# Optimization experiments

Hardware: AMD Instinct MI355X
Metric: run time of the kernel (lower is better)

Reference implementation:

```python
import jax, jax.numpy as jnp
import numpy as np

EPS = 1e-8  # torch.nn.CosineSimilarity default eps


def setup_inputs() -> dict:
    key = jax.random.key(0)
    k1, k2 = jax.random.split(key)
    B, C, D = 16384, 2048, 1024
    inputs = jax.random.normal(k1, (B, D), dtype=jnp.float32)
    class_avgs = jax.random.normal(k2, (C, D), dtype=jnp.float32)
    return {"inputs": inputs, "class_avgs": class_avgs}


def reference(inputs, class_avgs):
    # Pairwise cosine similarity: out[b, c] = <x_b, a_c> / (max(||x_b||, eps) * max(||a_c||, eps))
    x_norm = jnp.maximum(jnp.linalg.norm(inputs, axis=-1, keepdims=True), EPS)      # [B, 1]
    a_norm = jnp.maximum(jnp.linalg.norm(class_avgs, axis=-1, keepdims=True), EPS)  # [C, 1]
    xn = inputs / x_norm          # [B, D]
    an = class_avgs / a_norm      # [C, D]
    return jnp.einsum('bd,cd->bc', xn, an)  # [B, C]
```

## Files before the change

kernel.cpp:

```cpp
#include <hip/hip_runtime.h>
#include <stdint.h>


#define D_DIM 1024
#define N_DIM 2048
#define BMt 256
#define BNt 256
#define BKt 128
#define NKT 8

typedef int   i32x4 __attribute__((ext_vector_type(4)));
typedef float f32x4 __attribute__((ext_vector_type(4)));

__global__ __launch_bounds__(256) void quant_rows(
        const float* __restrict__ x, const float* __restrict__ a,
        char* __restrict__ xq, char* __restrict__ aq,
        float* __restrict__ sx, float* __restrict__ sa, int Bn) {
    const int blk = blockIdx.x;
    const float* in = (blk < Bn) ? x : a;
    char* outq      = (blk < Bn) ? xq : aq;
    float* outs     = (blk < Bn) ? sx : sa;
    const int row = (blk < Bn) ? blk : blk - Bn;
    const int t = threadIdx.x;
    const float4 v = ((const float4*)(in + (size_t)row * D_DIM))[t];
    float ss = v.x * v.x + v.y * v.y + v.z * v.z + v.w * v.w;
    float mx = fmaxf(fmaxf(fabsf(v.x), fabsf(v.y)), fmaxf(fabsf(v.z), fabsf(v.w)));
#pragma unroll
    for (int o = 1; o < 64; o <<= 1) {
        ss += __shfl_xor(ss, o);
        mx = fmaxf(mx, __shfl_xor(mx, o));
    }
    __shared__ float redS[4], redM[4];
    if ((t & 63) == 0) { redS[t >> 6] = ss; redM[t >> 6] = mx; }
    __syncthreads();
    const float tot  = redS[0] + redS[1] + redS[2] + redS[3];
    const float amax = fmaxf(fmaxf(redM[0], redM[1]), fmaxf(redM[2], redM[3]));
    const float inv  = (amax > 0.0f) ? (127.0f / amax) : 0.0f;
    int q0 = __float2int_rn(v.x * inv), q1 = __float2int_rn(v.y * inv);
    int q2 = __float2int_rn(v.z * inv), q3 = __float2int_rn(v.w * inv);
    q0 = min(127, max(-127, q0)); q1 = min(127, max(-127, q1));
    q2 = min(127, max(-127, q2)); q3 = min(127, max(-127, q3));
    char4 o; o.x = (char)q0; o.y = (char)q1; o.z = (char)q2; o.w = (char)q3;
    ((char4*)(outq + (size_t)row * D_DIM))[t] = o;
    if (t == 0) outs[row] = amax / (127.0f * fmaxf(sqrtf(tot), 1e-8f));
}

__device__ __forceinline__ void gload_lds16(const void* g, void* l) {
    __builtin_amdgcn_global_load_lds(
        (const __attribute__((address_space(1))) void*)g,
        (__attribute__((address_space(3))) void*)l,
        16, 0, 0);
}

#define BAR()     asm volatile("s_barrier" ::: "memory")
#define VMCNT0()  asm volatile("s_waitcnt vmcnt(0)" ::: "memory")

template<int P, bool STAGE>
__device__ __forceinline__ void ktile(
        int t,
        const unsigned char* __restrict__ sA,
        const unsigned char* __restrict__ sB,
        char* lds0, int dstW,
        const char* const (&pA)[2][2], const char* const (&pB)[2][2],
        i32x4 (&acc)[8][4])
{
    if constexpr (STAGE) {
        const int k1 = (t + 1) * BKt;
#pragma unroll
        for (int j = 0; j < 2; ++j) {
            gload_lds16(sA + (size_t)(j * 64) * D_DIM + k1,
                        lds0 + (P ^ 1) * 65536 + j * 8192 + dstW);
            gload_lds16(sA + (size_t)(128 + j * 64) * D_DIM + k1,
                        lds0 + (P ^ 1) * 65536 + 16384 + j * 8192 + dstW);
            gload_lds16(sB + (size_t)(j * 64) * D_DIM + k1,
                        lds0 + 32768 + (P ^ 1) * 65536 + j * 8192 + dstW);
            gload_lds16(sB + (size_t)(128 + j * 64) * D_DIM + k1,
                        lds0 + 32768 + (P ^ 1) * 65536 + 16384 + j * 8192 + dstW);
        }
    }

    i32x4 af[8][2], bf[4][2];
#pragma unroll
    for (int m = 0; m < 8; ++m)
#pragma unroll
        for (int kk = 0; kk < 2; ++kk)
            af[m][kk] = *(const i32x4*)(pA[P][kk] + m * 2048);
#pragma unroll
    for (int n = 0; n < 4; ++n)
#pragma unroll
        for (int kk = 0; kk < 2; ++kk)
            bf[n][kk] = *(const i32x4*)(pB[P][kk] + n * 2048);

    __builtin_amdgcn_s_setprio(1);
#pragma unroll
    for (int m = 0; m < 8; ++m)
#pragma unroll
        for (int n = 0; n < 4; ++n)
#pragma unroll
            for (int kk = 0; kk < 2; ++kk)
                acc[m][n] = __builtin_amdgcn_mfma_i32_16x16x64_i8(
                    af[m][kk], bf[n][kk], acc[m][n], 0, 0, 0);
    __builtin_amdgcn_s_setprio(0);

    if constexpr (STAGE) {
        VMCNT0();
        BAR();
    }
}

__global__ __launch_bounds__(512, 2) void gemm256(
        const unsigned char* __restrict__ A,
        const unsigned char* __restrict__ Bm,
        const float* __restrict__ sx,
        const float* __restrict__ sb,
        float* __restrict__ Cg)
{
    __shared__ char lds0[131072];

    const int nwg = gridDim.x;
    const int cpx = nwg >> 3;
    const int wg  = ((int)blockIdx.x & 7) * cpx + ((int)blockIdx.x >> 3);
    const int bm  = wg >> 3;
    const int bn  = wg & 7;
    const int rowA0 = bm * BMt;
    const int rowB0 = bn * BNt;

    const int tid  = threadIdx.x;
    const int lane = tid & 63;
    const int wid  = tid >> 6;
    const int wr   = wid >> 2;
    const int wc   = wid & 3;
    const int rl = lane & 15, ts = lane >> 4, r7 = rl & 7;

    const int swz0 = ((ts ^ r7) << 4);
    const int swz1 = (((4 + ts) ^ r7) << 4);
    const int aRow = (wr * 128 + rl) * 128;
    const int bRow = (wc * 64 + rl) * 128;
    const char* pA[2][2];
    const char* pB[2][2];
#pragma unroll
    for (int p = 0; p < 2; ++p) {
        pA[p][0] = lds0 + p * 65536 + aRow + swz0;
        pA[p][1] = lds0 + p * 65536 + aRow + swz1;
        pB[p][0] = lds0 + 32768 + p * 65536 + bRow + swz0;
        pB[p][1] = lds0 + 32768 + p * 65536 + bRow + swz1;
    }

    const int gcol = (((tid & 7) ^ ((tid >> 3) & 7)) << 4);
    const int grow = (tid >> 3);
    const unsigned char* sA = A  + (size_t)(rowA0 + grow) * D_DIM + gcol;
    const unsigned char* sB = Bm + (size_t)(rowB0 + grow) * D_DIM + gcol;
    const int dstW = wid * 1024;

    i32x4 acc[8][4] = {};

#pragma unroll
    for (int j = 0; j < 2; ++j) {
        gload_lds16(sA + (size_t)(j * 64) * D_DIM,        lds0 + j * 8192 + dstW);
        gload_lds16(sA + (size_t)(128 + j * 64) * D_DIM,  lds0 + 16384 + j * 8192 + dstW);
        gload_lds16(sB + (size_t)(j * 64) * D_DIM,        lds0 + 32768 + j * 8192 + dstW);
        gload_lds16(sB + (size_t)(128 + j * 64) * D_DIM,  lds0 + 32768 + 16384 + j * 8192 + dstW);
    }
    VMCNT0();
    BAR();

#pragma unroll 1
    for (int t = 0; t < NKT - 2; t += 2) {
        ktile<0, true>(t,     sA, sB, lds0, dstW, pA, pB, acc);
        ktile<1, true>(t + 1, sA, sB, lds0, dstW, pA, pB, acc);
    }
    ktile<0, true >(NKT - 2, sA, sB, lds0, dstW, pA, pB, acc);
    ktile<1, false>(NKT - 1, sA, sB, lds0, dstW, pA, pB, acc);

    const int crow0 = rowA0 + wr * 128 + ts * 4;
    const int ccol0 = rowB0 + wc * 64 + rl;
    float sbv[4];
#pragma unroll
    for (int n = 0; n < 4; ++n) sbv[n] = sb[ccol0 + n * 16];
#pragma unroll
    for (int m = 0; m < 8; ++m)
#pragma unroll
        for (int j = 0; j < 4; ++j) {
            const int row = crow0 + m * 16 + j;
            const float sav = sx[row];
#pragma unroll
            for (int n = 0; n < 4; ++n)
                Cg[(size_t)row * N_DIM + ccol0 + n * 16]
                    = (float)acc[m][n][j] * sav * sbv[n];
        }
}

extern "C" void kernel_launch(void* const* d_in, const int* in_sizes, int n_in,
                              void* d_out, int out_size, void* d_ws, size_t ws_size,
                              hipStream_t stream) {
    const float* x = (const float*)d_in[0];
    const float* a = (const float*)d_in[1];
    float* out = (float*)d_out;

    const int Bn = in_sizes[0] / D_DIM;
    const int Cn = in_sizes[1] / D_DIM;

    char*  xq = (char*)d_ws;
    char*  aq = xq + (size_t)Bn * D_DIM;
    float* sx = (float*)(aq + (size_t)Cn * D_DIM);
    float* sa = sx + Bn;

    quant_rows<<<Bn + Cn, 256, 0, stream>>>(x, a, xq, aq, sx, sa, Bn);

    const int grid = (Bn / BMt) * (Cn / BNt);
    gemm256<<<grid, 512, 0, stream>>>((const unsigned char*)xq,
                                      (const unsigned char*)aq, sx, sa, out);
}
```

Measured before the change: 69.25 us.

## Load B fragments directly from global, halve LDS, remap tiles and use nontemporal stores

```diff
diff --git a/kernel.cpp b/kernel.cpp
--- a/kernel.cpp
+++ b/kernel.cpp
@@ -9,17 +9,16 @@
 #define BKt 128
 #define NKT 8
 
-typedef int   i32x4 __attribute__((ext_vector_type(4)));
-typedef float f32x4 __attribute__((ext_vector_type(4)));
+typedef int i32x4 __attribute__((ext_vector_type(4)));
 
 __global__ __launch_bounds__(256) void quant_rows(
         const float* __restrict__ x, const float* __restrict__ a,
-        char* __restrict__ xq, char* __restrict__ aq,
+        signed char* __restrict__ xq, signed char* __restrict__ aq,
         float* __restrict__ sx, float* __restrict__ sa, int Bn) {
     const int blk = blockIdx.x;
-    const float* in = (blk < Bn) ? x : a;
-    char* outq      = (blk < Bn) ? xq : aq;
-    float* outs     = (blk < Bn) ? sx : sa;
+    const float* in   = (blk < Bn) ? x : a;
+    signed char* outq = (blk < Bn) ? xq : aq;
+    float* outs       = (blk < Bn) ? sx : sa;
     const int row = (blk < Bn) ? blk : blk - Bn;
     const int t = threadIdx.x;
     const float4 v = ((const float4*)(in + (size_t)row * D_DIM))[t];
@@ -58,10 +57,10 @@
 template<int P, bool STAGE>
 __device__ __forceinline__ void ktile(
         int t,
-        const unsigned char* __restrict__ sA,
-        const unsigned char* __restrict__ sB,
+        const signed char* __restrict__ sA,
+        const signed char* const (&bBase)[4],
         char* lds0, int dstW,
-        const char* const (&pA)[2][2], const char* const (&pB)[2][2],
+        const char* const (&pA)[2][2],
         i32x4 (&acc)[8][4])
 {
     if constexpr (STAGE) {
@@ -69,27 +68,25 @@
 #pragma unroll
         for (int j = 0; j < 2; ++j) {
             gload_lds16(sA + (size_t)(j * 64) * D_DIM + k1,
-                        lds0 + (P ^ 1) * 65536 + j * 8192 + dstW);
+                        lds0 + (P ^ 1) * 32768 + j * 8192 + dstW);
             gload_lds16(sA + (size_t)(128 + j * 64) * D_DIM + k1,
-                        lds0 + (P ^ 1) * 65536 + 16384 + j * 8192 + dstW);
-            gload_lds16(sB + (size_t)(j * 64) * D_DIM + k1,
-                        lds0 + 32768 + (P ^ 1) * 65536 + j * 8192 + dstW);
-            gload_lds16(sB + (size_t)(128 + j * 64) * D_DIM + k1,
-                        lds0 + 32768 + (P ^ 1) * 65536 + 16384 + j * 8192 + dstW);
+                        lds0 + (P ^ 1) * 32768 + 16384 + j * 8192 + dstW);
         }
     }
 
-    i32x4 af[8][2], bf[4][2];
+    i32x4 bf[4][2];
+#pragma unroll
+    for (int n = 0; n < 4; ++n)
+#pragma unroll
+        for (int kk = 0; kk < 2; ++kk)
+            bf[n][kk] = *(const i32x4*)(bBase[n] + t * BKt + kk * 64);
+
+    i32x4 af[8][2];
 #pragma unroll
     for (int m = 0; m < 8; ++m)
 #pragma unroll
         for (int kk = 0; kk < 2; ++kk)
             af[m][kk] = *(const i32x4*)(pA[P][kk] + m * 2048);
-#pragma unroll
-    for (int n = 0; n < 4; ++n)
-#pragma unroll
-        for (int kk = 0; kk < 2; ++kk)
-            bf[n][kk] = *(const i32x4*)(pB[P][kk] + n * 2048);
 
     __builtin_amdgcn_s_setprio(1);
 #pragma unroll
@@ -109,19 +106,19 @@
 }
 
 __global__ __launch_bounds__(512, 2) void gemm256(
-        const unsigned char* __restrict__ A,
-        const unsigned char* __restrict__ Bm,
+        const signed char* __restrict__ A,
+        const signed char* __restrict__ Bm,
         const float* __restrict__ sx,
         const float* __restrict__ sb,
         float* __restrict__ Cg)
 {
-    __shared__ char lds0[131072];
+    __shared__ char lds0[65536];
 
     const int nwg = gridDim.x;
     const int cpx = nwg >> 3;
     const int wg  = ((int)blockIdx.x & 7) * cpx + ((int)blockIdx.x >> 3);
-    const int bm  = wg >> 3;
-    const int bn  = wg & 7;
+    const int bn  = wg >> 6;
+    const int bm  = wg & 63;
     const int rowA0 = bm * BMt;
     const int rowB0 = bn * BNt;
 
@@ -135,42 +132,40 @@
     const int swz0 = ((ts ^ r7) << 4);
     const int swz1 = (((4 + ts) ^ r7) << 4);
     const int aRow = (wr * 128 + rl) * 128;
-    const int bRow = (wc * 64 + rl) * 128;
     const char* pA[2][2];
-    const char* pB[2][2];
 #pragma unroll
     for (int p = 0; p < 2; ++p) {
-        pA[p][0] = lds0 + p * 65536 + aRow + swz0;
-        pA[p][1] = lds0 + p * 65536 + aRow + swz1;
-        pB[p][0] = lds0 + 32768 + p * 65536 + bRow + swz0;
-        pB[p][1] = lds0 + 32768 + p * 65536 + bRow + swz1;
-    }
+        pA[p][0] = lds0 + p * 32768 + aRow + swz0;
+        pA[p][1] = lds0 + p * 32768 + aRow + swz1;
+    }
+
+    const signed char* bBase[4];
+#pragma unroll
+    for (int n = 0; n < 4; ++n)
+        bBase[n] = Bm + (size_t)(rowB0 + wc * 64 + n * 16 + rl) * D_DIM + ts * 16;
 
     const int gcol = (((tid & 7) ^ ((tid >> 3) & 7)) << 4);
     const int grow = (tid >> 3);
-    const unsigned char* sA = A  + (size_t)(rowA0 + grow) * D_DIM + gcol;
-    const unsigned char* sB = Bm + (size_t)(rowB0 + grow) * D_DIM + gcol;
+    const signed char* sA = A + (size_t)(rowA0 + grow) * D_DIM + gcol;
     const int dstW = wid * 1024;
 
     i32x4 acc[8][4] = {};
 
 #pragma unroll
     for (int j = 0; j < 2; ++j) {
-        gload_lds16(sA + (size_t)(j * 64) * D_DIM,        lds0 + j * 8192 + dstW);
-        gload_lds16(sA + (size_t)(128 + j * 64) * D_DIM,  lds0 + 16384 + j * 8192 + dstW);
-        gload_lds16(sB + (size_t)(j * 64) * D_DIM,        lds0 + 32768 + j * 8192 + dstW);
-        gload_lds16(sB + (size_t)(128 + j * 64) * D_DIM,  lds0 + 32768 + 16384 + j * 8192 + dstW);
+        gload_lds16(sA + (size_t)(j * 64) * D_DIM,       lds0 + j * 8192 + dstW);
+        gload_lds16(sA + (size_t)(128 + j * 64) * D_DIM, lds0 + 16384 + j * 8192 + dstW);
     }
     VMCNT0();
     BAR();
 
 #pragma unroll 1
     for (int t = 0; t < NKT - 2; t += 2) {
-        ktile<0, true>(t,     sA, sB, lds0, dstW, pA, pB, acc);
-        ktile<1, true>(t + 1, sA, sB, lds0, dstW, pA, pB, acc);
-    }
-    ktile<0, true >(NKT - 2, sA, sB, lds0, dstW, pA, pB, acc);
-    ktile<1, false>(NKT - 1, sA, sB, lds0, dstW, pA, pB, acc);
+        ktile<0, true>(t,     sA, bBase, lds0, dstW, pA, acc);
+        ktile<1, true>(t + 1, sA, bBase, lds0, dstW, pA, acc);
+    }
+    ktile<0, true >(NKT - 2, sA, bBase, lds0, dstW, pA, acc);
+    ktile<1, false>(NKT - 1, sA, bBase, lds0, dstW, pA, acc);
 
     const int crow0 = rowA0 + wr * 128 + ts * 4;
     const int ccol0 = rowB0 + wc * 64 + rl;
@@ -185,8 +180,9 @@
             const float sav = sx[row];
 #pragma unroll
             for (int n = 0; n < 4; ++n)
-                Cg[(size_t)row * N_DIM + ccol0 + n * 16]
-                    = (float)acc[m][n][j] * sav * sbv[n];
+                __builtin_nontemporal_store(
+                    (float)acc[m][n][j] * sav * sbv[n],
+                    &Cg[(size_t)row * N_DIM + ccol0 + n * 16]);
         }
 }
 
@@ -200,14 +196,13 @@
     const int Bn = in_sizes[0] / D_DIM;
     const int Cn = in_sizes[1] / D_DIM;
 
-    char*  xq = (char*)d_ws;
-    char*  aq = xq + (size_t)Bn * D_DIM;
+    signed char* xq = (signed char*)d_ws;
+    signed char* aq = xq + (size_t)Bn * D_DIM;
     float* sx = (float*)(aq + (size_t)Cn * D_DIM);
     float* sa = sx + Bn;
 
     quant_rows<<<Bn + Cn, 256, 0, stream>>>(x, a, xq, aq, sx, sa, Bn);
 
     const int grid = (Bn / BMt) * (Cn / BNt);
-    gemm256<<<grid, 512, 0, stream>>>((const unsigned char*)xq,
-                                      (const unsigned char*)aq, sx, sa, out);
-}
+    gemm256<<<grid, 512, 0, stream>>>(xq, aq, sx, sa, out);
+}
```

After: 101.6 us. +46.6%, slower.
